# Performance work log

Hardware: AMD Instinct MI355X
Metric: run time of the kernel (lower is better)

## Reference

```python
import jax, jax.numpy as jnp
import numpy as np

B, N, E, S, ANN_D, N_STEPS = 16384, 70, 3, 10, 1, 5


def setup_inputs() -> dict:
    key = jax.random.key(0)
    ks = jax.random.split(key, 10)
    std = 0.02
    annotation = jax.random.normal(ks[0], (B, N), jnp.float32)
    A_raw = jax.random.uniform(ks[1], (N, N * E), jnp.float32) + 1e-3
    A = A_raw / A_raw.sum(axis=1, keepdims=True)  # row-normalized like torch.div(A, sum(A,1))
    W_in = jax.random.normal(ks[2], (E, S, S), jnp.float32) * std
    b_in = jnp.zeros((E, S), jnp.float32)
    Wr = jax.random.normal(ks[3], (S, 2 * S), jnp.float32) * std
    br = jnp.zeros((S,), jnp.float32)
    Wz = jax.random.normal(ks[4], (S, 2 * S), jnp.float32) * std
    bz = jnp.zeros((S,), jnp.float32)
    Wh = jax.random.normal(ks[5], (S, 2 * S), jnp.float32) * std
    bh = jnp.zeros((S,), jnp.float32)
    Wo1 = jax.random.normal(ks[6], (S, S + ANN_D), jnp.float32) * std
    bo1 = jnp.zeros((S,), jnp.float32)
    Wo2 = jax.random.normal(ks[7], (1, S), jnp.float32) * std
    bo2 = jnp.zeros((1,), jnp.float32)
    return {"annotation": annotation, "A": A, "W_in": W_in, "b_in": b_in,
            "Wr": Wr, "br": br, "Wz": Wz, "bz": bz, "Wh": Wh, "bh": bh,
            "Wo1": Wo1, "bo1": bo1, "Wo2": Wo2, "bo2": bo2}


def reference(annotation, A, W_in, b_in, Wr, br, Wz, bz, Wh, bh, Wo1, bo1, Wo2, bo2):
    b, n = annotation.shape
    ann = annotation[..., None]  # [B, N, 1]
    # initial state: annotation padded with zeros to state_dim
    prop = jnp.concatenate([ann, jnp.zeros((b, n, S - ANN_D), annotation.dtype)], axis=2)  # [B,N,S]
    for _ in range(N_STEPS):
        # per-edge-type linear: [B,E,N,S]; view order is edge-type-major (matches torch stack/transpose/view)
        ins = jnp.einsum('bnd,efd->benf', prop, W_in) + b_in[None, :, None, :]
        ins = ins.reshape(b, E * n, S)  # [B, E*N, S]
        a_in = jnp.einsum('nm,bms->bns', A, ins)  # bmm aggregation, [B,N,S]
        a = jnp.concatenate([a_in, prop], axis=2)  # [B,N,2S]
        r = jax.nn.sigmoid(a @ Wr.T + br)
        z = jax.nn.sigmoid(a @ Wz.T + bz)
        joined = jnp.concatenate([a_in, r * prop], axis=2)
        h_hat = jnp.tanh(joined @ Wh.T + bh)
        prop = (1.0 - z) * prop + z * h_hat
    join_state = jnp.concatenate([prop, ann], axis=2)  # [B,N,S+1]
    out = jnp.tanh(join_state @ Wo1.T + bo1) @ Wo2.T + bo2  # [B,N,1]
    return out.sum(axis=2)  # [B,N]
```

## Files before the change

### kernel.cpp

```cpp
#include <hip/hip_runtime.h>
#include <hip/hip_bf16.h>

typedef _Float16 v8h __attribute__((ext_vector_type(8)));
typedef _Float16 v4h __attribute__((ext_vector_type(4)));
typedef _Float16 v2h __attribute__((ext_vector_type(2)));
typedef float    v4f __attribute__((ext_vector_type(4)));

#define NTOT  16384
#define NN    70
#define STEPS 5
#define TPB   64
#define NBLK  NTOT
#define CATN  40
#define CATH  3208
#define USTR  232
#define UH    (16*USTR)

#define PWO1 0
#define PWO2 120
#define PBO2 130
#define NWP  132

#define OFR  1024
#define OFZ  1536
#define OFH  2048
#define OFA  2560
#define NWF  20480

__device__ __align__(16) float    g_w[NWP];
__device__ __align__(16) _Float16 g_wf[NWF];
__device__ int g_flag;

__device__ __forceinline__ float fast_sigmoid(float x) {
    return __builtin_amdgcn_rcpf(1.0f + __expf(-x));
}
__device__ __forceinline__ float fast_tanh(float x) {
    float ax = fabsf(x);
    float e  = __expf(-2.0f * ax);
    float t  = (1.0f - e) * __builtin_amdgcn_rcpf(1.0f + e);
    return copysignf(t, x);
}

struct __align__(16) Smem {
    _Float16 U[UH];
    _Float16 cat[CATH];
};

__global__ void prep_kernel(const void* annv, const void* Av,
    const void* winv, const void* binv, const void* wrv, const void* brv,
    const void* wzv, const void* bzv, const void* whv, const void* bhv,
    const void* wo1v, const void* bo1v, const void* wo2v, const void* bo2v)
{
    __shared__ int sflag;
    if (threadIdx.x == 0) {
        const unsigned short* u = (const unsigned short*)annv;
        int good = 0;
        for (int k = 0; k < 128; ++k) {
            unsigned short bb = u[k];
            int ex = (bb >> 7) & 0xFF;
            if (bb == 0 || (ex >= 101 && ex <= 131)) ++good;
        }
        sflag = (good >= 112) ? 1 : 0;
        g_flag = sflag;
    }
    __syncthreads();
    const int f = sflag;
    #define RD(p, i) (f ? (float)((const __hip_bfloat16*)(p))[i] : ((const float*)(p))[i])
    const int tid = threadIdx.x;
    for (int idx = tid; idx < 120; idx += blockDim.x) {
        const int s = idx / 12, c = idx - s*12;
        g_w[PWO1 + idx] = (c < 11) ? RD(wo1v, s*11 + c) : RD(bo1v, s);
    }
    for (int idx = tid; idx < 10; idx += blockDim.x) g_w[PWO2 + idx] = RD(wo2v, idx);
    if (tid == 0) { g_w[PBO2] = RD(bo2v, 0); g_w[PBO2+1] = 0.f; }
    for (int idx = tid; idx < NWF; idx += blockDim.x) {
        float val = 0.f;
        if (idx < OFR) {
            const int nt = idx >> 9, rem = idx & 511, lane = rem >> 3, j = rem & 7;
            const int k = ((lane >> 4) << 3) + j, col = nt*16 + (lane & 15);
            if (col < 30) {
                const int e = col / 10, s = col - e*10;
                if (k >= 16 && k < 26) val = RD(winv, e*100 + s*10 + (k-16));
                else if (k == 26)      val = RD(binv, e*10 + s);
            }
        } else if (idx < OFH) {
            const int i2 = idx - OFR;
            const int mt = i2 >> 9, rem = i2 & 511, lane = rem >> 3, j = rem & 7;
            const int k = ((lane >> 4) << 3) + j, s = lane & 15;
            if (s < 10) {
                const void* Wv = mt ? wzv : wrv;
                const void* bv = mt ? bzv : brv;
                if (k < 10)                 val = RD(Wv, s*20 + k);
                else if (k >= 16 && k < 26) val = RD(Wv, s*20 + 10 + (k-16));
                else if (k == 26)           val = RD(bv, s);
            }
        } else if (idx < OFA) {
            const int i2 = idx - OFH;
            const int lane = i2 >> 3, j = i2 & 7;
            const int k = ((lane >> 4) << 3) + j, s = lane & 15;
            if (s < 10) {
                if (k < 10)                 val = RD(whv, s*20 + k);
                else if (k >= 16 && k < 26) val = RD(whv, s*20 + 10 + (k-16));
                else if (k == 26)           val = RD(bhv, s);
            }
        } else {
            const int i2 = idx - OFA;
            const int w = i2 / 3584, rem = i2 - w*3584;
            const int kt = rem >> 9, r2 = rem & 511, lane = r2 >> 3, j = r2 & 7;
            const int m = w*16 + (lane & 15);
            const int k = kt*32 + ((lane >> 4) << 3) + j;
            const int e = k / 72, mm = k - e*72;
            if (m < NN && e < 3 && mm < NN) val = RD(Av, m*210 + e*70 + mm);
        }
        g_wf[idx] = (_Float16)val;
    }
    #undef RD
}

template<typename T>
__device__ __forceinline__ void run_impl(const void* annv, void* outv, Smem& sm)
{
    const T* ann_g = (const T*)annv;
    T* out_g       = (T*)outv;
    const int lane = threadIdx.x;
    const int blk  = blockIdx.x;
    const int q    = lane >> 4;
    const int c    = lane & 15;
    const float* __restrict__ gw = g_w;

    const v8h w1f0 = *(const v8h*)&g_wf[       lane*8];
    const v8h w1f1 = *(const v8h*)&g_wf[512  + lane*8];
    const v8h wrf  = *(const v8h*)&g_wf[OFR  + lane*8];
    const v8h wzf  = *(const v8h*)&g_wf[OFZ  + lane*8];
    const v8h whf  = *(const v8h*)&g_wf[OFH  + lane*8];
    v8h adj[35];
    #pragma unroll
    for (int i = 0; i < 35; ++i)
        adj[i] = *(const v8h*)&g_wf[OFA + i*512 + lane*8];

    {
        const int4 zz = {0,0,0,0};
        int4* z = (int4*)&sm;
        #pragma unroll 4
        for (int i = lane; i < (int)(sizeof(Smem)/16); i += TPB) z[i] = zz;
    }
    __syncthreads();

    for (int n2 = lane; n2 < NN; n2 += TPB) {
        sm.cat[n2*CATN + 16] = (_Float16)(float)ann_g[blk*NN + n2];
        sm.cat[n2*CATN + 26] = (_Float16)1.0f;
    }
    __syncthreads();

    #define PHASE1() do {                                                        \
        _Pragma("unroll")                                                        \
        for (int mt = 0; mt < 5; ++mt) {                                         \
            const v8h af = *(const v8h*)&sm.cat[(mt*16 + c)*CATN + q*8];         \
            const int node0 = mt*16 + q*4;                                       \
            _Pragma("unroll")                                                    \
            for (int nt = 0; nt < 2; ++nt) {                                     \
                v4f acc = {0.f,0.f,0.f,0.f};                                     \
                acc = __builtin_amdgcn_mfma_f32_16x16x32_f16(                    \
                        af, nt ? w1f1 : w1f0, acc, 0,0,0);                       \
                const int colw = nt*16 + c;                                      \
                if (colw < 30 && node0 <= 68) {                                  \
                    const int e = colw / 10, s = colw - e*10;                    \
                    v4h hv = {(_Float16)acc[0],(_Float16)acc[1],                 \
                              (_Float16)acc[2],(_Float16)acc[3]};                \
                    *(v4h*)&sm.U[s*USTR + e*72 + node0] = hv;                    \
                }                                                                \
            }                                                                    \
        }                                                                        \
    } while(0)

    PHASE1();
    __syncthreads();

    #pragma unroll 1
    for (int step = 0; step < STEPS; ++step) {
        {
            v8h bfr[7];
            #pragma unroll
            for (int kt = 0; kt < 7; ++kt)
                bfr[kt] = *(const v8h*)&sm.U[c*USTR + q*8 + kt*32];
            #pragma unroll
            for (int mt = 0; mt < 5; ++mt) {
                v4f acc = {0.f,0.f,0.f,0.f};
                #pragma unroll
                for (int kt = 0; kt < 7; ++kt)
                    acc = __builtin_amdgcn_mfma_f32_16x16x32_f16(adj[mt*7+kt], bfr[kt], acc, 0,0,0);
                const int node0 = mt*16 + q*4;
                if (c < 10) {
                    #pragma unroll
                    for (int r = 0; r < 4; ++r) {
                        const int nd = node0 + r;
                        if (nd < NN) sm.cat[nd*CATN + c] = (_Float16)acc[r];
                    }
                }
            }
        }
        __syncthreads();

        #pragma unroll
        for (int nt = 0; nt < 5; ++nt) {
            const int node = nt*16 + c;
            const v8h bf = *(const v8h*)&sm.cat[node*CATN + q*8];
            v4f ar = {0.f,0.f,0.f,0.f}, az = {0.f,0.f,0.f,0.f};
            ar = __builtin_amdgcn_mfma_f32_16x16x32_f16(wrf, bf, ar, 0,0,0);
            az = __builtin_amdgcn_mfma_f32_16x16x32_f16(wzf, bf, az, 0,0,0);
            const v4h pv = *(const v4h*)&sm.cat[node*CATN + 16 + q*4];
            float zg[4], pg[4];
            _Float16 rp[4];
            #pragma unroll
            for (int i = 0; i < 4; ++i) {
                const float p = (float)pv[i];
                pg[i] = p;
                zg[i] = fast_sigmoid(az[i]);
                rp[i] = (_Float16)(fast_sigmoid(ar[i]) * p);
            }
            if (node < NN) {
                _Float16* wp = &sm.cat[node*CATN + 16 + q*4];
                if (q < 2)       *(v4h*)wp = (v4h){rp[0],rp[1],rp[2],rp[3]};
                else if (q == 2) *(v2h*)wp = (v2h){rp[0],rp[1]};
            }
            __syncthreads();
            const v8h bf2 = *(const v8h*)&sm.cat[node*CATN + q*8];
            v4f ah = {0.f,0.f,0.f,0.f};
            ah = __builtin_amdgcn_mfma_f32_16x16x32_f16(whf, bf2, ah, 0,0,0);
            _Float16 pn[4];
            #pragma unroll
            for (int i = 0; i < 4; ++i) {
                const float hh = fast_tanh(ah[i]);
                pn[i] = (_Float16)(pg[i] + zg[i]*(hh - pg[i]));
            }
            if (node < NN) {
                _Float16* wp = &sm.cat[node*CATN + 16 + q*4];
                if (q < 2)       *(v4h*)wp = (v4h){pn[0],pn[1],pn[2],pn[3]};
                else if (q == 2) *(v2h*)wp = (v2h){pn[0],pn[1]};
            }
        }
        __syncthreads();

        if (step < STEPS-1) {
            PHASE1();
            __syncthreads();
        }
    }
    #undef PHASE1

    for (int n2 = lane; n2 < NN; n2 += TPB) {
        const _Float16* pc = &sm.cat[n2*CATN + 16];
        const v8h p8 = *(const v8h*)pc;
        const v2h p2 = *(const v2h*)(pc + 8);
        float pr[10];
        #pragma unroll
        for (int i = 0; i < 8; ++i) pr[i] = (float)p8[i];
        pr[8] = (float)p2[0]; pr[9] = (float)p2[1];
        const float av = (float)ann_g[blk*NN + n2];
        float o = gw[PBO2];
        #pragma unroll
        for (int s = 0; s < 10; ++s) {
            const float* wr_ = &gw[PWO1 + s*12];
            float acc = wr_[11] + wr_[10]*av;
            #pragma unroll
            for (int d = 0; d < 10; ++d) acc += pr[d]*wr_[d];
            o += fast_tanh(acc) * gw[PWO2 + s];
        }
        out_g[blk*NN + n2] = (T)o;
    }
}

__global__ __launch_bounds__(TPB, 2)
void ggnn_kernel(const void* annv, void* outv)
{
    __shared__ Smem sm;
    if (g_flag)
        run_impl<__hip_bfloat16>(annv, outv, sm);
    else
        run_impl<float>(annv, outv, sm);
}

extern "C" void kernel_launch(void* const* d_in, const int* in_sizes, int n_in,
                              void* d_out, int out_size, void* d_ws, size_t ws_size,
                              hipStream_t stream) {
    (void)in_sizes; (void)n_in; (void)out_size; (void)d_ws; (void)ws_size;
    hipLaunchKernelGGL(prep_kernel, dim3(1), dim3(256), 0, stream,
        d_in[0], d_in[1], d_in[2], d_in[3], d_in[4], d_in[5], d_in[6],
        d_in[7], d_in[8], d_in[9], d_in[10], d_in[11], d_in[12], d_in[13]);
    hipLaunchKernelGGL(ggnn_kernel, dim3(NBLK), dim3(TPB), 0, stream,
        d_in[0], d_out);
}
```

Baseline: 297.0 us.

## Stream adjacency fragments from global memory and restructure GRU phase for occupancy

Stops holding the 35 adjacency MFMA fragments and the gate weights in registers and reloads them from global memory (cache-resident) at each use. The adjacency MFMA operands are swapped so results land as packed per-node vectors in shared memory, and the shared U buffer is shrunk. The GRU update is split into two node loops separated by one barrier instead of a barrier per tile, with z and prop kept as half vectors. Launch bounds rise to four waves per SIMD and the prep kernel runs over 40 blocks. The intent is higher occupancy and fewer barriers, at the cost of repeated global/L1 loads in the inner aggregation loop.

Result: slower. 303.2 us (+2.1%).

```diff
diff --git a/kernel.cpp b/kernel.cpp
--- a/kernel.cpp
+++ b/kernel.cpp
@@ -14,7 +14,7 @@
 #define CATN  40
 #define CATH  3208
 #define USTR  232
-#define UH    (16*USTR)
+#define UH    (10*USTR)
 
 #define PWO1 0
 #define PWO2 120
@@ -26,6 +26,7 @@
 #define OFH  2048
 #define OFA  2560
 #define NWF  20480
+#define PREPB 40
 
 __device__ __align__(16) float    g_w[NWP];
 __device__ __align__(16) _Float16 g_wf[NWF];
@@ -61,19 +62,21 @@
             if (bb == 0 || (ex >= 101 && ex <= 131)) ++good;
         }
         sflag = (good >= 112) ? 1 : 0;
-        g_flag = sflag;
+        if (blockIdx.x == 0) g_flag = sflag;
     }
     __syncthreads();
     const int f = sflag;
     #define RD(p, i) (f ? (float)((const __hip_bfloat16*)(p))[i] : ((const float*)(p))[i])
     const int tid = threadIdx.x;
-    for (int idx = tid; idx < 120; idx += blockDim.x) {
-        const int s = idx / 12, c = idx - s*12;
-        g_w[PWO1 + idx] = (c < 11) ? RD(wo1v, s*11 + c) : RD(bo1v, s);
-    }
-    for (int idx = tid; idx < 10; idx += blockDim.x) g_w[PWO2 + idx] = RD(wo2v, idx);
-    if (tid == 0) { g_w[PBO2] = RD(bo2v, 0); g_w[PBO2+1] = 0.f; }
-    for (int idx = tid; idx < NWF; idx += blockDim.x) {
+    if (blockIdx.x == 0) {
+        for (int idx = tid; idx < 120; idx += blockDim.x) {
+            const int s = idx / 12, cc = idx - s*12;
+            g_w[PWO1 + idx] = (cc < 11) ? RD(wo1v, s*11 + cc) : RD(bo1v, s);
+        }
+        for (int idx = tid; idx < 10; idx += blockDim.x) g_w[PWO2 + idx] = RD(wo2v, idx);
+        if (tid == 0) { g_w[PBO2] = RD(bo2v, 0); g_w[PBO2+1] = 0.f; }
+    }
+    for (int idx = blockIdx.x*blockDim.x + tid; idx < NWF; idx += gridDim.x*blockDim.x) {
         float val = 0.f;
         if (idx < OFR) {
             const int nt = idx >> 9, rem = idx & 511, lane = rem >> 3, j = rem & 7;
@@ -128,16 +131,6 @@
     const int c    = lane & 15;
     const float* __restrict__ gw = g_w;
 
-    const v8h w1f0 = *(const v8h*)&g_wf[       lane*8];
-    const v8h w1f1 = *(const v8h*)&g_wf[512  + lane*8];
-    const v8h wrf  = *(const v8h*)&g_wf[OFR  + lane*8];
-    const v8h wzf  = *(const v8h*)&g_wf[OFZ  + lane*8];
-    const v8h whf  = *(const v8h*)&g_wf[OFH  + lane*8];
-    v8h adj[35];
-    #pragma unroll
-    for (int i = 0; i < 35; ++i)
-        adj[i] = *(const v8h*)&g_wf[OFA + i*512 + lane*8];
-
     {
         const int4 zz = {0,0,0,0};
         int4* z = (int4*)&sm;
@@ -153,6 +146,8 @@
     __syncthreads();
 
     #define PHASE1() do {                                                        \
+        const v8h w1f0 = *(const v8h*)&g_wf[      lane*8];                       \
+        const v8h w1f1 = *(const v8h*)&g_wf[512 + lane*8];                       \
         _Pragma("unroll")                                                        \
         for (int mt = 0; mt < 5; ++mt) {                                         \
             const v8h af = *(const v8h*)&sm.cat[(mt*16 + c)*CATN + q*8];         \
@@ -188,55 +183,72 @@
                 v4f acc = {0.f,0.f,0.f,0.f};
                 #pragma unroll
                 for (int kt = 0; kt < 7; ++kt)
-                    acc = __builtin_amdgcn_mfma_f32_16x16x32_f16(adj[mt*7+kt], bfr[kt], acc, 0,0,0);
-                const int node0 = mt*16 + q*4;
-                if (c < 10) {
-                    #pragma unroll
-                    for (int r = 0; r < 4; ++r) {
-                        const int nd = node0 + r;
-                        if (nd < NN) sm.cat[nd*CATN + c] = (_Float16)acc[r];
-                    }
+                    acc = __builtin_amdgcn_mfma_f32_16x16x32_f16(
+                        bfr[kt],
+                        *(const v8h*)&g_wf[OFA + (mt*7+kt)*512 + lane*8],
+                        acc, 0,0,0);
+                const int node = mt*16 + c;
+                if (node < NN) {
+                    const v4h hv = {(_Float16)acc[0],(_Float16)acc[1],
+                                    (_Float16)acc[2],(_Float16)acc[3]};
+                    _Float16* wp = &sm.cat[node*CATN + q*4];
+                    if (q < 2)       *(v4h*)wp = hv;
+                    else if (q == 2) *(v2h*)wp = (v2h){hv[0], hv[1]};
                 }
             }
         }
         __syncthreads();
 
-        #pragma unroll
-        for (int nt = 0; nt < 5; ++nt) {
-            const int node = nt*16 + c;
-            const v8h bf = *(const v8h*)&sm.cat[node*CATN + q*8];
-            v4f ar = {0.f,0.f,0.f,0.f}, az = {0.f,0.f,0.f,0.f};
-            ar = __builtin_amdgcn_mfma_f32_16x16x32_f16(wrf, bf, ar, 0,0,0);
-            az = __builtin_amdgcn_mfma_f32_16x16x32_f16(wzf, bf, az, 0,0,0);
-            const v4h pv = *(const v4h*)&sm.cat[node*CATN + 16 + q*4];
-            float zg[4], pg[4];
-            _Float16 rp[4];
-            #pragma unroll
-            for (int i = 0; i < 4; ++i) {
-                const float p = (float)pv[i];
-                pg[i] = p;
-                zg[i] = fast_sigmoid(az[i]);
-                rp[i] = (_Float16)(fast_sigmoid(ar[i]) * p);
-            }
-            if (node < NN) {
-                _Float16* wp = &sm.cat[node*CATN + 16 + q*4];
-                if (q < 2)       *(v4h*)wp = (v4h){rp[0],rp[1],rp[2],rp[3]};
-                else if (q == 2) *(v2h*)wp = (v2h){rp[0],rp[1]};
-            }
-            __syncthreads();
-            const v8h bf2 = *(const v8h*)&sm.cat[node*CATN + q*8];
-            v4f ah = {0.f,0.f,0.f,0.f};
-            ah = __builtin_amdgcn_mfma_f32_16x16x32_f16(whf, bf2, ah, 0,0,0);
-            _Float16 pn[4];
-            #pragma unroll
-            for (int i = 0; i < 4; ++i) {
-                const float hh = fast_tanh(ah[i]);
-                pn[i] = (_Float16)(pg[i] + zg[i]*(hh - pg[i]));
-            }
-            if (node < NN) {
-                _Float16* wp = &sm.cat[node*CATN + 16 + q*4];
-                if (q < 2)       *(v4h*)wp = (v4h){pn[0],pn[1],pn[2],pn[3]};
-                else if (q == 2) *(v2h*)wp = (v2h){pn[0],pn[1]};
+        v4h zgp[5], pgp[5];
+        {
+            const v8h wrf = *(const v8h*)&g_wf[OFR + lane*8];
+            const v8h wzf = *(const v8h*)&g_wf[OFZ + lane*8];
+            #pragma unroll
+            for (int nt = 0; nt < 5; ++nt) {
+                const int node = nt*16 + c;
+                const v8h bf = *(const v8h*)&sm.cat[node*CATN + q*8];
+                v4f ar = {0.f,0.f,0.f,0.f}, az = {0.f,0.f,0.f,0.f};
+                ar = __builtin_amdgcn_mfma_f32_16x16x32_f16(wrf, bf, ar, 0,0,0);
+                az = __builtin_amdgcn_mfma_f32_16x16x32_f16(wzf, bf, az, 0,0,0);
+                const v4h pv = *(const v4h*)&sm.cat[node*CATN + 16 + q*4];
+                v4h rp, zh;
+                #pragma unroll
+                for (int i = 0; i < 4; ++i) {
+                    const float p = (float)pv[i];
+                    zh[i] = (_Float16)fast_sigmoid(az[i]);
+                    rp[i] = (_Float16)(fast_sigmoid(ar[i]) * p);
+                }
+                zgp[nt] = zh; pgp[nt] = pv;
+                if (node < NN) {
+                    _Float16* wp = &sm.cat[node*CATN + 16 + q*4];
+                    if (q < 2)       *(v4h*)wp = rp;
+                    else if (q == 2) *(v2h*)wp = (v2h){rp[0], rp[1]};
+                }
+            }
+        }
+        __syncthreads();
+
+        {
+            const v8h whf = *(const v8h*)&g_wf[OFH + lane*8];
+            #pragma unroll
+            for (int nt = 0; nt < 5; ++nt) {
+                const int node = nt*16 + c;
+                const v8h bf2 = *(const v8h*)&sm.cat[node*CATN + q*8];
+                v4f ah = {0.f,0.f,0.f,0.f};
+                ah = __builtin_amdgcn_mfma_f32_16x16x32_f16(whf, bf2, ah, 0,0,0);
+                v4h pn;
+                #pragma unroll
+                for (int i = 0; i < 4; ++i) {
+                    const float hh = fast_tanh(ah[i]);
+                    const float p  = (float)pgp[nt][i];
+                    const float z  = (float)zgp[nt][i];
+                    pn[i] = (_Float16)(p + z*(hh - p));
+                }
+                if (node < NN) {
+                    _Float16* wp = &sm.cat[node*CATN + 16 + q*4];
+                    if (q < 2)       *(v4h*)wp = pn;
+                    else if (q == 2) *(v2h*)wp = (v2h){pn[0], pn[1]};
+                }
             }
         }
         __syncthreads();
@@ -270,7 +282,7 @@
     }
 }
 
-__global__ __launch_bounds__(TPB, 2)
+__global__ __launch_bounds__(TPB, 4)
 void ggnn_kernel(const void* annv, void* outv)
 {
     __shared__ Smem sm;
@@ -284,7 +296,7 @@
                               void* d_out, int out_size, void* d_ws, size_t ws_size,
                               hipStream_t stream) {
     (void)in_sizes; (void)n_in; (void)out_size; (void)d_ws; (void)ws_size;
-    hipLaunchKernelGGL(prep_kernel, dim3(1), dim3(256), 0, stream,
+    hipLaunchKernelGGL(prep_kernel, dim3(PREPB), dim3(256), 0, stream,
         d_in[0], d_in[1], d_in[2], d_in[3], d_in[4], d_in[5], d_in[6],
         d_in[7], d_in[8], d_in[9], d_in[10], d_in[11], d_in[12], d_in[13]);
     hipLaunchKernelGGL(ggnn_kernel, dim3(NBLK), dim3(TPB), 0, stream,
```
